# Performance work log

Measured on AMD Instinct MI355X. Metric: run time of the kernel, lower is better.

The kernel has to match this reference:

```python
import jax, jax.numpy as jnp
import numpy as np

B, D_IN, T = 16, 1024, 1024
K, D_CB = 8192, 256
DECAY = 0.99
COMMITMENT = 0.15
CODEBOOK_LOSS_W = 1.0
THRESHOLD_DEAD = 2.0


def setup_inputs() -> dict:
    key = jax.random.key(0)
    ks = jax.random.split(key, 9)
    z = jax.random.normal(ks[0], (B, D_IN, T), dtype=jnp.float32)
    # weight-normed 1x1 conv params (kernel size 1 -> treat as matrices)
    in_v = jax.random.normal(ks[1], (D_CB, D_IN), dtype=jnp.float32) * 0.02
    in_g = jnp.ones((D_CB,), dtype=jnp.float32)
    in_b = jnp.zeros((D_CB,), dtype=jnp.float32)
    out_v = jax.random.normal(ks[2], (D_IN, D_CB), dtype=jnp.float32) * 0.02
    out_g = jnp.ones((D_IN,), dtype=jnp.float32)
    out_b = jnp.zeros((D_IN,), dtype=jnp.float32)
    codebook = jax.random.normal(ks[3], (K, D_CB), dtype=jnp.float32)
    cluster_size = jax.random.uniform(ks[4], (K,), dtype=jnp.float32) * 10.0
    return {"z": z, "in_g": in_g, "in_v": in_v, "in_b": in_b,
            "out_g": out_g, "out_v": out_v, "out_b": out_b,
            "codebook": codebook, "cluster_size": cluster_size}


def _wn_weight(g, v):
    # weight_norm dim=0: per-output-channel L2 norm over remaining dims
    return g[:, None] * v / jnp.linalg.norm(v, axis=1, keepdims=True)


def _l2norm(x, axis=-1, eps=1e-12):
    return x / jnp.maximum(jnp.linalg.norm(x, axis=axis, keepdims=True), eps)


def reference(z, in_g, in_v, in_b, out_g, out_v, out_b, codebook, cluster_size):
    sg = jax.lax.stop_gradient
    # in_project: 1x1 weight-normed conv  [B, D_IN, T] -> [B, D_CB, T]
    w_in = _wn_weight(in_g, in_v)
    z_e = jnp.einsum('oi,bit->bot', w_in, z) + in_b[None, :, None]

    # decode_latents
    enc = z_e.transpose(0, 2, 1).reshape(-1, D_CB)           # [(B*T), D_CB]
    enc_n = _l2norm(enc)
    cb_n = _l2norm(codebook)
    dist = (jnp.sum(enc_n ** 2, axis=1, keepdims=True)
            - 2.0 * enc_n @ cb_n.T
            + jnp.sum(cb_n ** 2, axis=1)[None, :])           # [(B*T), K]
    flat_idx = jnp.argmax(-dist, axis=1)                      # [(B*T)]
    indices = flat_idx.reshape(B, T)                          # [B, T]
    z_q = codebook[indices].transpose(0, 2, 1)                # [B, D_CB, T]

    # perplexity / usage stats (one-hot mean == normalized counts)
    n_tokens = B * T
    counts = jnp.zeros((K,), dtype=z_e.dtype).at[flat_idx].add(1.0)
    avg_probs = counts / n_tokens
    perplexity = jnp.exp(-jnp.sum(avg_probs * jnp.log(avg_probs + 1e-10)))

    # EMA cluster-size update (training, forced_activation=False): functional
    new_cluster_size = cluster_size * DECAY + counts * (1.0 - DECAY)
    active_num = jnp.sum(new_cluster_size > THRESHOLD_DEAD).astype(jnp.float32)

    # losses (training path)
    commit_loss = jnp.mean((z_e - sg(z_q)) ** 2, axis=(1, 2)) * COMMITMENT
    codebook_loss = jnp.mean((z_q - sg(z_e)) ** 2, axis=(1, 2)) * CODEBOOK_LOSS_W

    # straight-through
    z_q_st = z_e + sg(z_q - z_e)

    # out_project: 1x1 weight-normed conv  [B, D_CB, T] -> [B, D_IN, T]
    w_out = _wn_weight(out_g, out_v)
    z_q_out = jnp.einsum('oi,bit->bot', w_out, z_q_st) + out_b[None, :, None]

    return (z_q_out, indices, commit_loss, codebook_loss, dist, perplexity, active_num)
```

## Files before the change

kernel.cpp:

```cpp
#include <hip/hip_runtime.h>
#include <stdint.h>

#define B_    16
#define D_IN_ 1024
#define T_    1024
#define K_    8192
#define D_CB_ 256
#define NTOK  (B_*T_)

#define WS_WIN   0
#define WS_WOUT  262144
#define WS_ENC   524288
#define WS_INVE  4718592
#define WS_ESQ   4734976
#define WS_INVC  4751360
#define WS_CSQ   4759552
#define WS_KEYS  4767744
#define WS_CNT   4800512
#define WS_LOSS  4808704

#define OUT_ZQ   0
#define OUT_IDX  16777216
#define OUT_COMM 16793600
#define OUT_CB   16793616
#define OUT_DIST 16793632
#define OUT_PERP 151011360
#define OUT_ACT  151011361

__device__ __forceinline__ float wave_sum(float s) {
    for (int o = 32; o; o >>= 1) s += __shfl_down(s, o, 64);
    return s;
}

__global__ void wn_kernel(const float* __restrict__ g, const float* __restrict__ v,
                          float* __restrict__ w, int rows, int cols) {
    int wave = threadIdx.x >> 6, lane = threadIdx.x & 63;
    int row = blockIdx.x * 4 + wave;
    if (row >= rows) return;
    const float* vr = v + (size_t)row * cols;
    float s = 0.f;
    for (int c = lane; c < (cols >> 2); c += 64) {
        float4 x = ((const float4*)vr)[c];
        s += x.x*x.x + x.y*x.y + x.z*x.z + x.w*x.w;
    }
    s = wave_sum(s);
    s = __shfl(s, 0, 64);
    float norm = sqrtf(s);
    float gr = g[row];
    float* wr = w + (size_t)row * cols;
    for (int c = lane; c < cols; c += 64)
        wr[c] = gr * vr[c] / norm;
}

__global__ void rownorm_kernel(const float* __restrict__ x, float* __restrict__ inv,
                               float* __restrict__ sq) {
    int wave = threadIdx.x >> 6, lane = threadIdx.x & 63;
    int row = blockIdx.x * 4 + wave;
    float4 v = ((const float4*)(x + (size_t)row * D_CB_))[lane];
    float s = v.x*v.x + v.y*v.y + v.z*v.z + v.w*v.w;
    s = wave_sum(s);
    if (lane == 0) {
        float n = fmaxf(sqrtf(s), 1e-12f);
        float iv = 1.0f / n;
        inv[row] = iv;
        sq[row]  = s * iv * iv;
    }
}

__global__ __launch_bounds__(256) void ze_gemm(const float* __restrict__ w,
        const float* __restrict__ z, const float* __restrict__ bias,
        float* __restrict__ enc) {
    __shared__ float As[32 * 68];
    __shared__ float Bs[32 * 68];
    int b  = blockIdx.z;
    int o0 = blockIdx.y * 64;
    int t0 = blockIdx.x * 64;
    int t  = threadIdx.x;
    int tx = t & 15, ty = t >> 4;
    float acc[4][4] = {};
    const float* zb = z + (size_t)b * D_IN_ * T_;
    for (int kt = 0; kt < D_IN_ / 32; ++kt) {
        #pragma unroll
        for (int p = 0; p < 2; ++p) {
            int q = p * 256 + t;
            int r = q >> 3, c4 = q & 7;
            float4 x = *(const float4*)&w[(size_t)(o0 + r) * D_IN_ + kt * 32 + c4 * 4];
            As[(c4*4+0)*68 + r] = x.x; As[(c4*4+1)*68 + r] = x.y;
            As[(c4*4+2)*68 + r] = x.z; As[(c4*4+3)*68 + r] = x.w;
        }
        #pragma unroll
        for (int p = 0; p < 2; ++p) {
            int q = p * 256 + t;
            int r = q >> 4, c4 = q & 15;
            float4 x = *(const float4*)&zb[(size_t)(kt * 32 + r) * T_ + t0 + c4 * 4];
            *(float4*)&Bs[r * 68 + c4 * 4] = x;
        }
        __syncthreads();
        #pragma unroll 4
        for (int k = 0; k < 32; ++k) {
            float a[4], bv[4];
            *(float4*)a  = *(float4*)&As[k * 68 + tx * 4];
            *(float4*)bv = *(float4*)&Bs[k * 68 + ty * 4];
            #pragma unroll
            for (int i = 0; i < 4; ++i)
                #pragma unroll
                for (int j = 0; j < 4; ++j)
                    acc[i][j] = fmaf(a[j], bv[i], acc[i][j]);
        }
        __syncthreads();
    }
    float bias4[4];
    *(float4*)bias4 = *(const float4*)&bias[o0 + tx * 4];
    #pragma unroll
    for (int i = 0; i < 4; ++i) {
        int token = b * T_ + t0 + ty * 4 + i;
        float4 v = make_float4(acc[i][0] + bias4[0], acc[i][1] + bias4[1],
                               acc[i][2] + bias4[2], acc[i][3] + bias4[3]);
        *(float4*)&enc[(size_t)token * D_CB_ + o0 + tx * 4] = v;
    }
}

#define DLD 132
__global__ __launch_bounds__(256) void dist_gemm(
        const float* __restrict__ enc, const float* __restrict__ inve,
        const float* __restrict__ esq, const float* __restrict__ cb,
        const float* __restrict__ invc, const float* __restrict__ csq,
        float* __restrict__ dist, unsigned long long* __restrict__ keys) {
    __shared__ float As[32 * DLD];
    __shared__ float Bs[32 * DLD];
    int c0 = blockIdx.x * 128;
    int r0 = blockIdx.y * 128;
    int t  = threadIdx.x;
    int tx = t & 15, ty = t >> 4;
    float acc[8][8] = {};
    for (int kt = 0; kt < D_CB_ / 32; ++kt) {
        #pragma unroll
        for (int p = 0; p < 4; ++p) {
            int q = p * 256 + t;
            int r = q >> 3, c4 = q & 7;
            float iv = inve[r0 + r];
            float4 x = *(const float4*)&enc[(size_t)(r0 + r) * D_CB_ + kt * 32 + c4 * 4];
            As[(c4*4+0)*DLD + r] = x.x * iv; As[(c4*4+1)*DLD + r] = x.y * iv;
            As[(c4*4+2)*DLD + r] = x.z * iv; As[(c4*4+3)*DLD + r] = x.w * iv;
        }
        #pragma unroll
        for (int p = 0; p < 4; ++p) {
            int q = p * 256 + t;
            int r = q >> 3, c4 = q & 7;
            float iv = invc[c0 + r];
            float4 x = *(const float4*)&cb[(size_t)(c0 + r) * D_CB_ + kt * 32 + c4 * 4];
            Bs[(c4*4+0)*DLD + r] = x.x * iv; Bs[(c4*4+1)*DLD + r] = x.y * iv;
            Bs[(c4*4+2)*DLD + r] = x.z * iv; Bs[(c4*4+3)*DLD + r] = x.w * iv;
        }
        __syncthreads();
        #pragma unroll 4
        for (int k = 0; k < 32; ++k) {
            float a[8], bv[8];
            *(float4*)&a[0]  = *(float4*)&As[k * DLD + ty * 4];
            *(float4*)&a[4]  = *(float4*)&As[k * DLD + 64 + ty * 4];
            *(float4*)&bv[0] = *(float4*)&Bs[k * DLD + tx * 4];
            *(float4*)&bv[4] = *(float4*)&Bs[k * DLD + 64 + tx * 4];
            #pragma unroll
            for (int i = 0; i < 8; ++i)
                #pragma unroll
                for (int j = 0; j < 8; ++j)
                    acc[i][j] = fmaf(a[i], bv[j], acc[i][j]);
        }
        __syncthreads();
    }
    float s1[8], s2[8];
    #pragma unroll
    for (int i = 0; i < 4; ++i) {
        s1[i]   = esq[r0 + ty * 4 + i];      s1[4+i] = esq[r0 + 64 + ty * 4 + i];
        s2[i]   = csq[c0 + tx * 4 + i];      s2[4+i] = csq[c0 + 64 + tx * 4 + i];
    }
    unsigned long long rmin[8];
    #pragma unroll
    for (int i = 0; i < 8; ++i) rmin[i] = ~0ull;
    #pragma unroll
    for (int i = 0; i < 8; ++i) {
        int row = r0 + (i < 4 ? ty * 4 + i : 64 + ty * 4 + (i - 4));
        float d[8];
        #pragma unroll
        for (int j = 0; j < 8; ++j) {
            d[j] = fmaf(-2.0f, acc[i][j], s1[i] + s2[j]);
            int col = c0 + (j < 4 ? tx * 4 + j : 64 + tx * 4 + (j - 4));
            unsigned long long key =
                ((unsigned long long)__float_as_uint(d[j]) << 32) | (unsigned int)col;
            rmin[i] = key < rmin[i] ? key : rmin[i];
        }
        *(float4*)&dist[(size_t)row * K_ + c0 + tx * 4]      = make_float4(d[0], d[1], d[2], d[3]);
        *(float4*)&dist[(size_t)row * K_ + c0 + 64 + tx * 4] = make_float4(d[4], d[5], d[6], d[7]);
    }
    __syncthreads();
    unsigned long long* red = (unsigned long long*)As;
    if (t < 128) red[t] = ~0ull;
    __syncthreads();
    #pragma unroll
    for (int i = 0; i < 8; ++i) {
        int rl = (i < 4 ? ty * 4 + i : 64 + ty * 4 + (i - 4));
        atomicMin(&red[rl], rmin[i]);
    }
    __syncthreads();
    if (t < 128) atomicMin(&keys[r0 + t], red[t]);
}

__global__ void token_kernel(const float* __restrict__ enc, const float* __restrict__ cb,
        const unsigned long long* __restrict__ keys, float* __restrict__ idx_out,
        float* __restrict__ counts, float* __restrict__ loss) {
    int wave = threadIdx.x >> 6, lane = threadIdx.x & 63;
    int tok = blockIdx.x * 4 + wave;
    int idx = (int)(unsigned int)(keys[tok] & 0xffffffffull);
    float4 e = ((const float4*)(enc + (size_t)tok * D_CB_))[lane];
    float4 q = ((const float4*)(cb  + (size_t)idx * D_CB_))[lane];
    float dx = e.x - q.x, dy = e.y - q.y, dz = e.z - q.z, dw = e.w - q.w;
    float s = dx*dx + dy*dy + dz*dz + dw*dw;
    s = wave_sum(s);
    if (lane == 0) {
        idx_out[tok] = (float)idx;
        atomicAdd(&counts[idx], 1.0f);
        atomicAdd(&loss[tok >> 10], s);
    }
}

__global__ __launch_bounds__(256) void out_gemm(const float* __restrict__ w,
        const float* __restrict__ cb, const unsigned long long* __restrict__ keys,
        const float* __restrict__ bias, float* __restrict__ out) {
    __shared__ float As[32 * 68];
    __shared__ float Bs[32 * 68];
    __shared__ int idxs[64];
    int b  = blockIdx.z;
    int d0 = blockIdx.y * 64;
    int t0 = blockIdx.x * 64;
    int t  = threadIdx.x;
    if (t < 64) idxs[t] = (int)(unsigned int)(keys[b * T_ + t0 + t] & 0xffffffffull);
    __syncthreads();
    int tx = t & 15, ty = t >> 4;
    float acc[4][4] = {};
    for (int kt = 0; kt < D_CB_ / 32; ++kt) {
        #pragma unroll
        for (int p = 0; p < 2; ++p) {
            int q = p * 256 + t;
            int r = q >> 3, c4 = q & 7;
            float4 x = *(const float4*)&w[(size_t)(d0 + r) * D_CB_ + kt * 32 + c4 * 4];
            As[(c4*4+0)*68 + r] = x.x; As[(c4*4+1)*68 + r] = x.y;
            As[(c4*4+2)*68 + r] = x.z; As[(c4*4+3)*68 + r] = x.w;
        }
        #pragma unroll
        for (int p = 0; p < 2; ++p) {
            int q = p * 256 + t;
            int r = q >> 3, c4 = q & 7;
            float4 x = *(const float4*)&cb[(size_t)idxs[r] * D_CB_ + kt * 32 + c4 * 4];
            Bs[(c4*4+0)*68 + r] = x.x; Bs[(c4*4+1)*68 + r] = x.y;
            Bs[(c4*4+2)*68 + r] = x.z; Bs[(c4*4+3)*68 + r] = x.w;
        }
        __syncthreads();
        #pragma unroll 4
        for (int k = 0; k < 32; ++k) {
            float a[4], bv[4];
            *(float4*)a  = *(float4*)&As[k * 68 + ty * 4];
            *(float4*)bv = *(float4*)&Bs[k * 68 + tx * 4];
            #pragma unroll
            for (int i = 0; i < 4; ++i)
                #pragma unroll
                for (int j = 0; j < 4; ++j)
                    acc[i][j] = fmaf(a[i], bv[j], acc[i][j]);
        }
        __syncthreads();
    }
    #pragma unroll
    for (int i = 0; i < 4; ++i) {
        int d = d0 + ty * 4 + i;
        float bb = bias[d];
        float4 v = make_float4(acc[i][0] + bb, acc[i][1] + bb, acc[i][2] + bb, acc[i][3] + bb);
        *(float4*)&out[(size_t)b * D_IN_ * T_ + (size_t)d * T_ + t0 + tx * 4] = v;
    }
}

__global__ void finalize_kernel(const float* __restrict__ counts, const float* __restrict__ cs,
                                const float* __restrict__ loss, float* __restrict__ out) {
    int t = threadIdx.x;
    float H = 0.f, act = 0.f;
    for (int k = t; k < K_; k += 256) {
        float c = counts[k];
        float p = c * (1.0f / 16384.0f);
        H += p * logf(p + 1e-10f);
        float ncs = cs[k] * 0.99f + c * 0.01f;
        if (ncs > 2.0f) act += 1.0f;
    }
    __shared__ float sh[8];
    for (int o = 32; o; o >>= 1) { H += __shfl_down(H, o, 64); act += __shfl_down(act, o, 64); }
    int wave = t >> 6, lane = t & 63;
    if (lane == 0) { sh[wave] = H; sh[4 + wave] = act; }
    __syncthreads();
    if (t == 0) {
        out[OUT_PERP] = expf(-(sh[0] + sh[1] + sh[2] + sh[3]));
        out[OUT_ACT]  = sh[4] + sh[5] + sh[6] + sh[7];
    }
    if (t < 16) {
        float m = loss[t] * (1.0f / 262144.0f);
        out[OUT_COMM + t] = m * 0.15f;
        out[OUT_CB + t]   = m;
    }
}

extern "C" void kernel_launch(void* const* d_in, const int* in_sizes, int n_in,
                              void* d_out, int out_size, void* d_ws, size_t ws_size,
                              hipStream_t stream) {
    const float* z        = (const float*)d_in[0];
    const float* in_g     = (const float*)d_in[1];
    const float* in_v     = (const float*)d_in[2];
    const float* in_b     = (const float*)d_in[3];
    const float* out_g    = (const float*)d_in[4];
    const float* out_v    = (const float*)d_in[5];
    const float* out_b    = (const float*)d_in[6];
    const float* codebook = (const float*)d_in[7];
    const float* cluster  = (const float*)d_in[8];
    float* out = (float*)d_out;
    float* ws  = (float*)d_ws;
    unsigned long long* keys = (unsigned long long*)(ws + WS_KEYS);

    hipMemsetAsync(keys, 0xFF, NTOK * sizeof(unsigned long long), stream);
    hipMemsetAsync(ws + WS_CNT, 0, (K_ + 16) * sizeof(float), stream);

    wn_kernel<<<64, 256, 0, stream>>>(in_g, in_v, ws + WS_WIN, D_CB_, D_IN_);
    wn_kernel<<<256, 256, 0, stream>>>(out_g, out_v, ws + WS_WOUT, D_IN_, D_CB_);
    rownorm_kernel<<<K_ / 4, 256, 0, stream>>>(codebook, ws + WS_INVC, ws + WS_CSQ);
    ze_gemm<<<dim3(16, 4, 16), 256, 0, stream>>>(ws + WS_WIN, z, in_b, ws + WS_ENC);
    rownorm_kernel<<<NTOK / 4, 256, 0, stream>>>(ws + WS_ENC, ws + WS_INVE, ws + WS_ESQ);
    dist_gemm<<<dim3(64, 128), 256, 0, stream>>>(ws + WS_ENC, ws + WS_INVE, ws + WS_ESQ,
                                                 codebook, ws + WS_INVC, ws + WS_CSQ,
                                                 out + OUT_DIST, keys);
    token_kernel<<<NTOK / 4, 256, 0, stream>>>(ws + WS_ENC, codebook, keys,
                                               out + OUT_IDX, ws + WS_CNT, ws + WS_LOSS);
    out_gemm<<<dim3(16, 16, 16), 256, 0, stream>>>(ws + WS_WOUT, codebook, keys,
                                                   out_b, out + OUT_ZQ);
    finalize_kernel<<<1, 256, 0, stream>>>(ws + WS_CNT, cluster, ws + WS_LOSS, out);
}
```

Baseline: 1.892 ms.

## Use split-bf16 MFMA for the distance GEMM with near-tie argmin fixup

Replaces the FP32 SIMT distance GEMM with MFMA bf16 instructions. Each normalized operand is split into hi and lo bf16 parts, and three products are accumulated to approximate FP32 accuracy. Each block writes its top-2 candidates per row, a separate reduction picks the argmin, and rows whose top two candidates fall within a margin are recomputed exactly in FP32. Scratch buffers reuse the z_q output region before it is written. This adds precision risk in the dist output and in argmin ties, plus extra launches and scratch traffic.

```diff
diff --git a/kernel.cpp b/kernel.cpp
--- a/kernel.cpp
+++ b/kernel.cpp
@@ -7,6 +7,10 @@
 #define K_    8192
 #define D_CB_ 256
 #define NTOK  (B_*T_)
+
+typedef unsigned long long ull;
+typedef __attribute__((ext_vector_type(8))) short short8;
+typedef __attribute__((ext_vector_type(4))) float f32x4;
 
 #define WS_WIN   0
 #define WS_WOUT  262144
@@ -27,9 +31,23 @@
 #define OUT_PERP 151011360
 #define OUT_ACT  151011361
 
+#define SCR_EHI  0
+#define SCR_ELO  2097152
+#define SCR_CHI  4194304
+#define SCR_CLO  5242880
+#define SCR_MINB 6291456
+#define SCR_FLAG 10485760
+
+#define MARGIN 2.5e-4f
+
 __device__ __forceinline__ float wave_sum(float s) {
     for (int o = 32; o; o >>= 1) s += __shfl_down(s, o, 64);
     return s;
+}
+
+__device__ __forceinline__ unsigned short f2bf(float f) {
+    unsigned u = __float_as_uint(f);
+    return (unsigned short)((u + 0x7fffu + ((u >> 16) & 1u)) >> 16);
 }
 
 __global__ void wn_kernel(const float* __restrict__ g, const float* __restrict__ v,
@@ -52,19 +70,28 @@
         wr[c] = gr * vr[c] / norm;
 }
 
-__global__ void rownorm_kernel(const float* __restrict__ x, float* __restrict__ inv,
-                               float* __restrict__ sq) {
+__global__ void split_kernel(const float* __restrict__ x, float* __restrict__ inv,
+                             float* __restrict__ sq, unsigned short* __restrict__ hi,
+                             unsigned short* __restrict__ lo) {
     int wave = threadIdx.x >> 6, lane = threadIdx.x & 63;
     int row = blockIdx.x * 4 + wave;
     float4 v = ((const float4*)(x + (size_t)row * D_CB_))[lane];
     float s = v.x*v.x + v.y*v.y + v.z*v.z + v.w*v.w;
     s = wave_sum(s);
-    if (lane == 0) {
-        float n = fmaxf(sqrtf(s), 1e-12f);
-        float iv = 1.0f / n;
-        inv[row] = iv;
-        sq[row]  = s * iv * iv;
-    }
+    s = __shfl(s, 0, 64);
+    float n = fmaxf(sqrtf(s), 1e-12f);
+    float iv = 1.0f / n;
+    if (lane == 0) { inv[row] = iv; sq[row] = s * iv * iv; }
+    float f[4] = { v.x*iv, v.y*iv, v.z*iv, v.w*iv };
+    unsigned short h[4], l[4];
+    #pragma unroll
+    for (int i = 0; i < 4; ++i) {
+        h[i] = f2bf(f[i]);
+        float hf = __uint_as_float((unsigned)h[i] << 16);
+        l[i] = f2bf(f[i] - hf);
+    }
+    *(ushort4*)(hi + (size_t)row * D_CB_ + lane * 4) = make_ushort4(h[0], h[1], h[2], h[3]);
+    *(ushort4*)(lo + (size_t)row * D_CB_ + lane * 4) = make_ushort4(l[0], l[1], l[2], l[3]);
 }
 
 __global__ __launch_bounds__(256) void ze_gemm(const float* __restrict__ w,
@@ -120,93 +147,154 @@
     }
 }
 
-#define DLD 132
-__global__ __launch_bounds__(256) void dist_gemm(
-        const float* __restrict__ enc, const float* __restrict__ inve,
+__global__ __launch_bounds__(256, 3) void dist_mfma(
+        const unsigned short* __restrict__ ehi, const unsigned short* __restrict__ elo,
+        const unsigned short* __restrict__ chi, const unsigned short* __restrict__ clo,
+        const float* __restrict__ esq, const float* __restrict__ csq,
+        float* __restrict__ dist, ull* __restrict__ minb) {
+    __shared__ ull pairs[2][64][2][2];
+    int bid = blockIdx.x;
+    int lin = (bid & 7) * 1024 + (bid >> 3);
+    int bx = lin >> 7;
+    int by = lin & 127;
+    int r0 = by * 128, c0 = bx * 128;
+    int t = threadIdx.x;
+    int wave = t >> 6, lane = t & 63;
+    int wm = wave >> 1, wn = wave & 1;
+    int lr = lane & 15, kg = lane >> 4;
+
+    const unsigned short* ea = ehi + (size_t)(r0 + wm*64 + lr) * D_CB_ + kg*8;
+    const unsigned short* eb = elo + (size_t)(r0 + wm*64 + lr) * D_CB_ + kg*8;
+    const unsigned short* ca = chi + (size_t)(c0 + wn*64 + lr) * D_CB_ + kg*8;
+    const unsigned short* cl = clo + (size_t)(c0 + wn*64 + lr) * D_CB_ + kg*8;
+
+    f32x4 acc[4][4] = {};
+    for (int kt = 0; kt < D_CB_ / 32; ++kt) {
+        short8 ah[4], al[4], bh[4], bl[4];
+        int k = kt * 32;
+        #pragma unroll
+        for (int i = 0; i < 4; ++i) {
+            ah[i] = *(const short8*)(ea + (size_t)i*16*D_CB_ + k);
+            al[i] = *(const short8*)(eb + (size_t)i*16*D_CB_ + k);
+            bh[i] = *(const short8*)(ca + (size_t)i*16*D_CB_ + k);
+            bl[i] = *(const short8*)(cl + (size_t)i*16*D_CB_ + k);
+        }
+        #pragma unroll
+        for (int i = 0; i < 4; ++i)
+            #pragma unroll
+            for (int j = 0; j < 4; ++j) {
+                acc[i][j] = __builtin_amdgcn_mfma_f32_16x16x32_bf16(ah[i], bh[j], acc[i][j], 0, 0, 0);
+                acc[i][j] = __builtin_amdgcn_mfma_f32_16x16x32_bf16(ah[i], bl[j], acc[i][j], 0, 0, 0);
+                acc[i][j] = __builtin_amdgcn_mfma_f32_16x16x32_bf16(al[i], bh[j], acc[i][j], 0, 0, 0);
+            }
+    }
+    float csqv[4];
+    #pragma unroll
+    for (int j = 0; j < 4; ++j) csqv[j] = csq[c0 + wn*64 + j*16 + lr];
+    #pragma unroll
+    for (int i = 0; i < 4; ++i) {
+        #pragma unroll
+        for (int r = 0; r < 4; ++r) {
+            int rl = i*16 + kg*4 + r;
+            int grow = r0 + wm*64 + rl;
+            float es = esq[grow];
+            float* drow = dist + (size_t)grow * K_ + c0 + wn*64 + lr;
+            ull m1 = ~0ull, m2 = ~0ull;
+            #pragma unroll
+            for (int j = 0; j < 4; ++j) {
+                float d = fmaf(-2.0f, acc[i][j][r], es + csqv[j]);
+                drow[j*16] = d;
+                ull key = ((ull)__float_as_uint(d) << 32) | (unsigned)(c0 + wn*64 + j*16 + lr);
+                if (key < m1) { m2 = m1; m1 = key; } else if (key < m2) m2 = key;
+            }
+            #pragma unroll
+            for (int off = 1; off < 16; off <<= 1) {
+                ull o1 = __shfl_xor(m1, off, 64);
+                ull o2 = __shfl_xor(m2, off, 64);
+                ull n1 = o1 < m1 ? o1 : m1;
+                ull x  = o1 < m1 ? m1 : o1;
+                ull y  = o2 < m2 ? o2 : m2;
+                m2 = x < y ? x : y;
+                m1 = n1;
+            }
+            if (lr == 0) { pairs[wm][rl][wn][0] = m1; pairs[wm][rl][wn][1] = m2; }
+        }
+    }
+    __syncthreads();
+    if (t < 128) {
+        int wm2 = t >> 6, rl = t & 63;
+        ull a1 = pairs[wm2][rl][0][0], a2 = pairs[wm2][rl][0][1];
+        ull b1 = pairs[wm2][rl][1][0], b2 = pairs[wm2][rl][1][1];
+        ull m1 = a1 < b1 ? a1 : b1;
+        ull x  = a1 < b1 ? b1 : a1;
+        ull y  = a2 < b2 ? a2 : b2;
+        ull m2 = x < y ? x : y;
+        size_t grow = (size_t)(r0 + wm2*64 + rl);
+        minb[(grow*64 + bx)*2 + 0] = m1;
+        minb[(grow*64 + bx)*2 + 1] = m2;
+    }
+}
+
+__global__ void minreduce(const ull* __restrict__ minb, ull* __restrict__ keys,
+                          int* __restrict__ flags) {
+    int wave = threadIdx.x >> 6, lane = threadIdx.x & 63;
+    int row = blockIdx.x * 4 + wave;
+    ull m1 = minb[((size_t)row*64 + lane)*2 + 0];
+    ull m2 = minb[((size_t)row*64 + lane)*2 + 1];
+    #pragma unroll
+    for (int off = 1; off < 64; off <<= 1) {
+        ull o1 = __shfl_xor(m1, off, 64);
+        ull o2 = __shfl_xor(m2, off, 64);
+        ull n1 = o1 < m1 ? o1 : m1;
+        ull x  = o1 < m1 ? m1 : o1;
+        ull y  = o2 < m2 ? o2 : m2;
+        m2 = x < y ? x : y;
+        m1 = n1;
+    }
+    if (lane == 0) {
+        keys[row] = m1;
+        float d1 = __uint_as_float((unsigned)(m1 >> 32));
+        float d2 = __uint_as_float((unsigned)(m2 >> 32));
+        flags[row] = (d2 - d1 < MARGIN) ? 1 : 0;
+    }
+}
+
+__global__ void argmin_fix(const float* __restrict__ enc, const float* __restrict__ inve,
         const float* __restrict__ esq, const float* __restrict__ cb,
         const float* __restrict__ invc, const float* __restrict__ csq,
-        float* __restrict__ dist, unsigned long long* __restrict__ keys) {
-    __shared__ float As[32 * DLD];
-    __shared__ float Bs[32 * DLD];
-    int c0 = blockIdx.x * 128;
-    int r0 = blockIdx.y * 128;
-    int t  = threadIdx.x;
-    int tx = t & 15, ty = t >> 4;
-    float acc[8][8] = {};
-    for (int kt = 0; kt < D_CB_ / 32; ++kt) {
-        #pragma unroll
-        for (int p = 0; p < 4; ++p) {
-            int q = p * 256 + t;
-            int r = q >> 3, c4 = q & 7;
-            float iv = inve[r0 + r];
-            float4 x = *(const float4*)&enc[(size_t)(r0 + r) * D_CB_ + kt * 32 + c4 * 4];
-            As[(c4*4+0)*DLD + r] = x.x * iv; As[(c4*4+1)*DLD + r] = x.y * iv;
-            As[(c4*4+2)*DLD + r] = x.z * iv; As[(c4*4+3)*DLD + r] = x.w * iv;
-        }
-        #pragma unroll
-        for (int p = 0; p < 4; ++p) {
-            int q = p * 256 + t;
-            int r = q >> 3, c4 = q & 7;
-            float iv = invc[c0 + r];
-            float4 x = *(const float4*)&cb[(size_t)(c0 + r) * D_CB_ + kt * 32 + c4 * 4];
-            Bs[(c4*4+0)*DLD + r] = x.x * iv; Bs[(c4*4+1)*DLD + r] = x.y * iv;
-            Bs[(c4*4+2)*DLD + r] = x.z * iv; Bs[(c4*4+3)*DLD + r] = x.w * iv;
-        }
-        __syncthreads();
-        #pragma unroll 4
-        for (int k = 0; k < 32; ++k) {
-            float a[8], bv[8];
-            *(float4*)&a[0]  = *(float4*)&As[k * DLD + ty * 4];
-            *(float4*)&a[4]  = *(float4*)&As[k * DLD + 64 + ty * 4];
-            *(float4*)&bv[0] = *(float4*)&Bs[k * DLD + tx * 4];
-            *(float4*)&bv[4] = *(float4*)&Bs[k * DLD + 64 + tx * 4];
-            #pragma unroll
-            for (int i = 0; i < 8; ++i)
-                #pragma unroll
-                for (int j = 0; j < 8; ++j)
-                    acc[i][j] = fmaf(a[i], bv[j], acc[i][j]);
-        }
-        __syncthreads();
-    }
-    float s1[8], s2[8];
-    #pragma unroll
-    for (int i = 0; i < 4; ++i) {
-        s1[i]   = esq[r0 + ty * 4 + i];      s1[4+i] = esq[r0 + 64 + ty * 4 + i];
-        s2[i]   = csq[c0 + tx * 4 + i];      s2[4+i] = csq[c0 + 64 + tx * 4 + i];
-    }
-    unsigned long long rmin[8];
-    #pragma unroll
-    for (int i = 0; i < 8; ++i) rmin[i] = ~0ull;
-    #pragma unroll
-    for (int i = 0; i < 8; ++i) {
-        int row = r0 + (i < 4 ? ty * 4 + i : 64 + ty * 4 + (i - 4));
-        float d[8];
-        #pragma unroll
-        for (int j = 0; j < 8; ++j) {
-            d[j] = fmaf(-2.0f, acc[i][j], s1[i] + s2[j]);
-            int col = c0 + (j < 4 ? tx * 4 + j : 64 + tx * 4 + (j - 4));
-            unsigned long long key =
-                ((unsigned long long)__float_as_uint(d[j]) << 32) | (unsigned int)col;
-            rmin[i] = key < rmin[i] ? key : rmin[i];
-        }
-        *(float4*)&dist[(size_t)row * K_ + c0 + tx * 4]      = make_float4(d[0], d[1], d[2], d[3]);
-        *(float4*)&dist[(size_t)row * K_ + c0 + 64 + tx * 4] = make_float4(d[4], d[5], d[6], d[7]);
-    }
-    __syncthreads();
-    unsigned long long* red = (unsigned long long*)As;
-    if (t < 128) red[t] = ~0ull;
-    __syncthreads();
-    #pragma unroll
-    for (int i = 0; i < 8; ++i) {
-        int rl = (i < 4 ? ty * 4 + i : 64 + ty * 4 + (i - 4));
-        atomicMin(&red[rl], rmin[i]);
-    }
-    __syncthreads();
-    if (t < 128) atomicMin(&keys[r0 + t], red[t]);
+        const float* __restrict__ dist, const int* __restrict__ flags,
+        ull* __restrict__ keys) {
+    int row = blockIdx.x;
+    if (!flags[row]) return;
+    int lane = threadIdx.x;
+    ull k0 = keys[row];
+    float thr = __uint_as_float((unsigned)(k0 >> 32)) + MARGIN;
+    float iv = inve[row];
+    float4 ev = ((const float4*)(enc + (size_t)row * D_CB_))[lane];
+    ev.x *= iv; ev.y *= iv; ev.z *= iv; ev.w *= iv;
+    float es = esq[row];
+    float best = 1e30f; int bestc = 0;
+    for (int base = 0; base < K_; base += 64) {
+        float d = dist[(size_t)row * K_ + base + lane];
+        ull mask = __ballot(d <= thr);
+        while (mask) {
+            int b = __ffsll(mask) - 1;
+            mask &= mask - 1;
+            int c = base + b;
+            float4 cv = ((const float4*)(cb + (size_t)c * D_CB_))[lane];
+            float p = ev.x*cv.x + ev.y*cv.y + ev.z*cv.z + ev.w*cv.w;
+            p = wave_sum(p);
+            p = __shfl(p, 0, 64);
+            float dx = fmaf(-2.0f * invc[c], p, es + csq[c]);
+            if (dx < best) { best = dx; bestc = c; }
+        }
+    }
+    if (lane == 0)
+        keys[row] = ((ull)__float_as_uint(best) << 32) | (unsigned)bestc;
 }
 
 __global__ void token_kernel(const float* __restrict__ enc, const float* __restrict__ cb,
-        const unsigned long long* __restrict__ keys, float* __restrict__ idx_out,
+        const ull* __restrict__ keys, float* __restrict__ idx_out,
         float* __restrict__ counts, float* __restrict__ loss) {
     int wave = threadIdx.x >> 6, lane = threadIdx.x & 63;
     int tok = blockIdx.x * 4 + wave;
@@ -224,7 +312,7 @@
 }
 
 __global__ __launch_bounds__(256) void out_gemm(const float* __restrict__ w,
-        const float* __restrict__ cb, const unsigned long long* __restrict__ keys,
+        const float* __restrict__ cb, const ull* __restrict__ keys,
         const float* __restrict__ bias, float* __restrict__ out) {
     __shared__ float As[32 * 68];
     __shared__ float Bs[32 * 68];
@@ -318,19 +406,29 @@
     const float* cluster  = (const float*)d_in[8];
     float* out = (float*)d_out;
     float* ws  = (float*)d_ws;
-    unsigned long long* keys = (unsigned long long*)(ws + WS_KEYS);
-
-    hipMemsetAsync(keys, 0xFF, NTOK * sizeof(unsigned long long), stream);
+    ull* keys  = (ull*)(ws + WS_KEYS);
+
+    float* scr = out + OUT_ZQ;
+    unsigned short* ehi = (unsigned short*)(scr + SCR_EHI);
+    unsigned short* elo = (unsigned short*)(scr + SCR_ELO);
+    unsigned short* chi = (unsigned short*)(scr + SCR_CHI);
+    unsigned short* clo = (unsigned short*)(scr + SCR_CLO);
+    ull* minb  = (ull*)(scr + SCR_MINB);
+    int* flags = (int*)(scr + SCR_FLAG);
+
     hipMemsetAsync(ws + WS_CNT, 0, (K_ + 16) * sizeof(float), stream);
 
     wn_kernel<<<64, 256, 0, stream>>>(in_g, in_v, ws + WS_WIN, D_CB_, D_IN_);
     wn_kernel<<<256, 256, 0, stream>>>(out_g, out_v, ws + WS_WOUT, D_IN_, D_CB_);
-    rownorm_kernel<<<K_ / 4, 256, 0, stream>>>(codebook, ws + WS_INVC, ws + WS_CSQ);
+    split_kernel<<<K_ / 4, 256, 0, stream>>>(codebook, ws + WS_INVC, ws + WS_CSQ, chi, clo);
     ze_gemm<<<dim3(16, 4, 16), 256, 0, stream>>>(ws + WS_WIN, z, in_b, ws + WS_ENC);
-    rownorm_kernel<<<NTOK / 4, 256, 0, stream>>>(ws + WS_ENC, ws + WS_INVE, ws + WS_ESQ);
-    dist_gemm<<<dim3(64, 128), 256, 0, stream>>>(ws + WS_ENC, ws + WS_INVE, ws + WS_ESQ,
-                                                 codebook, ws + WS_INVC, ws + WS_CSQ,
-                                                 out + OUT_DIST, keys);
+    split_kernel<<<NTOK / 4, 256, 0, stream>>>(ws + WS_ENC, ws + WS_INVE, ws + WS_ESQ, ehi, elo);
+    dist_mfma<<<8192, 256, 0, stream>>>(ehi, elo, chi, clo, ws + WS_ESQ, ws + WS_CSQ,
+                                        out + OUT_DIST, minb);
+    minreduce<<<NTOK / 4, 256, 0, stream>>>(minb, keys, flags);
+    argmin_fix<<<NTOK, 64, 0, stream>>>(ws + WS_ENC, ws + WS_INVE, ws + WS_ESQ,
+                                        codebook, ws + WS_INVC, ws + WS_CSQ,
+                                        out + OUT_DIST, flags, keys);
     token_kernel<<<NTOK / 4, 256, 0, stream>>>(ws + WS_ENC, codebook, keys,
                                                out + OUT_IDX, ws + WS_CNT, ws + WS_LOSS);
     out_gemm<<<dim3(16, 16, 16), 256, 0, stream>>>(ws + WS_WOUT, codebook, keys,
```

After: 1.615 ms. 1.17x faster.
